# Kernel tuning notes

Hardware: AMD Instinct MI355X
Metric: run time of the kernel (lower is better)

The kernel has to match this reference:

```python
import jax, jax.numpy as jnp
import numpy as np

WIDTH_POW = 9
WIDTH = 2 ** WIDTH_POW          # 512
HALF = WIDTH // 2               # 256
DEPTH = 32
BATCH = 65536
EPS = 0.01


def setup_inputs() -> dict:
    key = jax.random.key(0)
    k1, k2, k3, k4, k5, k6 = jax.random.split(key, 6)
    X = jax.random.normal(k1, (BATCH, WIDTH), dtype=jnp.float32)
    # butterfly rotation angles, one stage of depth-1 butterfly per layer
    thetas = jax.random.uniform(k2, (DEPTH, HALF), dtype=jnp.float32) * (2.0 * np.pi)
    # SmoothBendActivation params, init uniform in [-eps, eps]
    def u(k):
        return jax.random.uniform(k, (DEPTH, WIDTH), dtype=jnp.float32) * (2 * EPS) - EPS
    biases = u(k3)
    slopes1 = u(k4)
    slopes2 = u(k5)
    curvatures = u(k6)
    return {"X": X, "thetas": thetas, "biases": biases,
            "slopes1": slopes1, "slopes2": slopes2, "curvatures": curvatures}


def reference(X, thetas, biases, slopes1, slopes2, curvatures):
    B = X.shape[0]

    def step(x, p):
        theta, bias, s1, s2, curv = p
        # --- orthogonal butterfly rotation (depth 1) ---
        c = jnp.cos(theta)  # [HALF]
        s = jnp.sin(theta)
        x0 = x[:, :HALF]
        x1 = x[:, HALF:]
        n0 = x0 * c + x1 * s
        n1 = -x0 * s + x1 * c
        # fixed permutation perm[2j] = j, perm[2j+1] = j + HALF: interleave n0, n1
        x = jnp.stack([n0, n1], axis=-1).reshape(B, WIDTH)
        # --- smooth bend activation ---
        m1 = jnp.exp(s1)
        m2 = jnp.exp(s2)
        a = (m1 + m2) * 0.5
        cc = (m2 - m1) / (2.0 * a)
        b = jnp.sinh(bias)
        k = jnp.exp(curv)
        u = x * a - b
        x = u + cc * jnp.sqrt(u * u + 1.0 / k)
        return x, None

    out, _ = jax.lax.scan(step, X, (thetas, biases, slopes1, slopes2, curvatures))
    return out  # num_outputs == WIDTH, so no final slice needed
```

## Files before the change

kernel.cpp:

```cpp
#include <hip/hip_runtime.h>
#include <math.h>

#define WIDTH 512
#define HALF  256
#define DEPTH 32
#define BATCH 65536
#define RPW   8

__device__ float4 g_T1[DEPTH * WIDTH];
__device__ float  g_T2[DEPTH * WIDTH];

__global__ __launch_bounds__(256) void precompute_kernel(
    const float* __restrict__ thetas, const float* __restrict__ biases,
    const float* __restrict__ slopes1, const float* __restrict__ slopes2,
    const float* __restrict__ curvatures) {
  int tid = blockIdx.x * 256 + threadIdx.x;
  if (tid >= DEPTH * WIDTH) return;
  int d = tid >> 9;
  int p = tid & 511;
  int rot = (d + 1) % 9;
  int j = ((p << rot) | (p >> (9 - rot))) & 511;
  int i = j >> 1;
  int role = j & 1;
  float th = thetas[d * HALF + i];
  float c = cosf(th), s = sinf(th);
  float m1 = expf(slopes1[d * WIDTH + j]);
  float m2 = expf(slopes2[d * WIDTH + j]);
  float a  = 0.5f * (m1 + m2);
  float cc = (m2 - m1) / (m1 + m2);
  float b  = sinhf(biases[d * WIDTH + j]);
  float invk = expf(-curvatures[d * WIDTH + j]);
  float A = a * c;
  float S = role ? (-a * s) : (a * s);
  int q = d * WIDTH + ((p & 7) * 64 + (p >> 3));
  g_T1[q] = make_float4(A, S, b, cc);
  g_T2[q] = invk;
}

#if __has_builtin(__builtin_amdgcn_sqrtf)
#define FAST_SQRT(x) __builtin_amdgcn_sqrtf(x)
#else
#define FAST_SQRT(x) sqrtf(x)
#endif

template <int M>
__device__ __forceinline__ float xshfl(float v) {
  if constexpr (M < 32) {
    constexpr int ctl = (M << 10) | 0x1F;
    return __int_as_float(__builtin_amdgcn_ds_swizzle(__float_as_int(v), ctl));
  } else {
    return __shfl_xor(v, 32, 64);
  }
}

__device__ __forceinline__ float stepf(float xs, float v, float4 P, float ik) {
  float u = fmaf(xs, P.x, fmaf(v, P.y, -P.z));
  float t = fmaf(u, u, ik);
  return fmaf(P.w, FAST_SQRT(t), u);
}

template <int K>
__device__ __forceinline__ void do_layer(const float4* __restrict__ t1,
                                         const float* __restrict__ t2,
                                         float (&x)[8][RPW]) {
  if constexpr (K >= 3) {
    constexpr int m = 1 << (K - 3);
#pragma unroll
    for (int s = 0; s < 8; ++s) {
      float4 P = t1[s * 64];
      float ik = t2[s * 64];
#pragma unroll
      for (int r = 0; r < RPW; ++r) {
        float xs = x[s][r];
        float v = xshfl<m>(xs);
        x[s][r] = stepf(xs, v, P, ik);
      }
    }
  } else {
    constexpr int SX = 1 << K;
#pragma unroll
    for (int s0 = 0; s0 < 8; ++s0) {
      if (s0 & SX) continue;
      const int s1 = s0 | SX;
      float4 P0 = t1[s0 * 64];
      float ik0 = t2[s0 * 64];
      float4 P1 = t1[s1 * 64];
      float ik1 = t2[s1 * 64];
#pragma unroll
      for (int r = 0; r < RPW; ++r) {
        float v0 = x[s0][r], v1 = x[s1][r];
        float n0 = stepf(v0, v1, P0, ik0);
        float n1 = stepf(v1, v0, P1, ik1);
        x[s0][r] = n0;
        x[s1][r] = n1;
      }
    }
  }
}

__global__ __launch_bounds__(256, 4) void net_kernel(const float* __restrict__ X,
                                                     float* __restrict__ out) {
  const int lane = threadIdx.x & 63;
  const int wv = blockIdx.x * 4 + (threadIdx.x >> 6);
  const size_t row0 = (size_t)wv * RPW;

  float x[8][RPW];
  const float4* __restrict__ Xv =
      reinterpret_cast<const float4*>(X + row0 * WIDTH);
#pragma unroll
  for (int r = 0; r < RPW; ++r) {
    float4 a = Xv[r * (WIDTH / 4) + lane * 2];
    float4 b = Xv[r * (WIDTH / 4) + lane * 2 + 1];
    x[0][r] = a.x; x[1][r] = a.y; x[2][r] = a.z; x[3][r] = a.w;
    x[4][r] = b.x; x[5][r] = b.y; x[6][r] = b.z; x[7][r] = b.w;
  }

#define RUN_LAYER(DD)                                                   \
  do {                                                                  \
    if (d0 + DD < DEPTH) {                                              \
      do_layer<8 - DD>(g_T1 + (d0 + DD) * WIDTH + lane,                 \
                       g_T2 + (d0 + DD) * WIDTH + lane, x);             \
    }                                                                   \
  } while (0)

  for (int d0 = 0; d0 < DEPTH; d0 += 9) {
    RUN_LAYER(0); RUN_LAYER(1); RUN_LAYER(2);
    RUN_LAYER(3); RUN_LAYER(4); RUN_LAYER(5);
    RUN_LAYER(6); RUN_LAYER(7); RUN_LAYER(8);
  }
#undef RUN_LAYER

  float* __restrict__ O = out + row0 * WIDTH;
#pragma unroll
  for (int s = 0; s < 8; ++s) {
    const int p = lane * 8 + s;
    const int cfin = ((p << 5) | (p >> 4)) & 511;
#pragma unroll
    for (int r = 0; r < RPW; ++r) O[r * WIDTH + cfin] = x[s][r];
  }
}

extern "C" void kernel_launch(void* const* d_in, const int* in_sizes, int n_in,
                              void* d_out, int out_size, void* d_ws, size_t ws_size,
                              hipStream_t stream) {
  const float* X          = (const float*)d_in[0];
  const float* thetas     = (const float*)d_in[1];
  const float* biases     = (const float*)d_in[2];
  const float* slopes1    = (const float*)d_in[3];
  const float* slopes2    = (const float*)d_in[4];
  const float* curvatures = (const float*)d_in[5];
  float* out = (float*)d_out;

  hipLaunchKernelGGL(precompute_kernel, dim3((DEPTH * WIDTH + 255) / 256),
                     dim3(256), 0, stream, thetas, biases, slopes1, slopes2,
                     curvatures);
  hipLaunchKernelGGL(net_kernel, dim3(BATCH / (RPW * 4)), dim3(256), 0, stream,
                     X, out);
}
```

Baseline: 202.5 us.

## Split each row across two wavefronts, exchanging via LDS for top bit

Each wavefront now holds 4 row elements per lane instead of 8. A 128-thread block covers one 8-row group, and the parameter table layout is remapped to match. The butterfly level that crosses wavefronts goes through shared memory with two __syncthreads per such layer. This halves register pressure per thread and doubles the wave count to improve occupancy and latency hiding, at the cost of LDS traffic and block barriers.

```diff
diff --git a/kernel.cpp b/kernel.cpp
--- a/kernel.cpp
+++ b/kernel.cpp
@@ -6,6 +6,7 @@
 #define DEPTH 32
 #define BATCH 65536
 #define RPW   8
+#define NS    4
 
 __device__ float4 g_T1[DEPTH * WIDTH];
 __device__ float  g_T2[DEPTH * WIDTH];
@@ -17,24 +18,25 @@
   int tid = blockIdx.x * 256 + threadIdx.x;
   if (tid >= DEPTH * WIDTH) return;
   int d = tid >> 9;
-  int p = tid & 511;
+  int idx = tid & 511;
+  int w = idx >> 8, s = (idx >> 6) & 3, l = idx & 63;
+  int p = w * 256 + l * 4 + s;
   int rot = (d + 1) % 9;
   int j = ((p << rot) | (p >> (9 - rot))) & 511;
   int i = j >> 1;
   int role = j & 1;
   float th = thetas[d * HALF + i];
-  float c = cosf(th), s = sinf(th);
+  float c = cosf(th), sn = sinf(th);
   float m1 = expf(slopes1[d * WIDTH + j]);
   float m2 = expf(slopes2[d * WIDTH + j]);
   float a  = 0.5f * (m1 + m2);
   float cc = (m2 - m1) / (m1 + m2);
   float b  = sinhf(biases[d * WIDTH + j]);
-  float invk = expf(-curvatures[d * WIDTH + j]);
+  float ik = expf(-curvatures[d * WIDTH + j]);
   float A = a * c;
-  float S = role ? (-a * s) : (a * s);
-  int q = d * WIDTH + ((p & 7) * 64 + (p >> 3));
-  g_T1[q] = make_float4(A, S, b, cc);
-  g_T2[q] = invk;
+  float S = role ? (-a * sn) : (a * sn);
+  g_T1[d * WIDTH + idx] = make_float4(A, S, b, cc);
+  g_T2[d * WIDTH + idx] = ik;
 }
 
 #if __has_builtin(__builtin_amdgcn_sqrtf)
@@ -60,13 +62,33 @@
 }
 
 template <int K>
-__device__ __forceinline__ void do_layer(const float4* __restrict__ t1,
-                                         const float* __restrict__ t2,
-                                         float (&x)[8][RPW]) {
-  if constexpr (K >= 3) {
-    constexpr int m = 1 << (K - 3);
+__device__ __forceinline__ void layer_step(const float4* __restrict__ t1,
+                                           const float* __restrict__ t2,
+                                           float (&x)[NS][RPW], float* xb,
+                                           int tid) {
+  if constexpr (K == 8) {
 #pragma unroll
-    for (int s = 0; s < 8; ++s) {
+    for (int s = 0; s < NS; ++s)
+#pragma unroll
+      for (int r = 0; r < RPW; ++r)
+        xb[(s * RPW + r) * 128 + tid] = x[s][r];
+    __syncthreads();
+    const int pt = tid ^ 64;
+#pragma unroll
+    for (int s = 0; s < NS; ++s) {
+      float4 P = t1[s * 64];
+      float ik = t2[s * 64];
+      float v[RPW];
+#pragma unroll
+      for (int r = 0; r < RPW; ++r) v[r] = xb[(s * RPW + r) * 128 + pt];
+#pragma unroll
+      for (int r = 0; r < RPW; ++r) x[s][r] = stepf(x[s][r], v[r], P, ik);
+    }
+    __syncthreads();
+  } else if constexpr (K >= 2) {
+    constexpr int m = 1 << (K - 2);
+#pragma unroll
+    for (int s = 0; s < NS; ++s) {
       float4 P = t1[s * 64];
       float ik = t2[s * 64];
 #pragma unroll
@@ -79,7 +101,7 @@
   } else {
     constexpr int SX = 1 << K;
 #pragma unroll
-    for (int s0 = 0; s0 < 8; ++s0) {
+    for (int s0 = 0; s0 < NS; ++s0) {
       if (s0 & SX) continue;
       const int s1 = s0 | SX;
       float4 P0 = t1[s0 * 64];
@@ -98,31 +120,32 @@
   }
 }
 
-__global__ __launch_bounds__(256, 4) void net_kernel(const float* __restrict__ X,
+__global__ __launch_bounds__(128, 4) void net_kernel(const float* __restrict__ X,
                                                      float* __restrict__ out) {
-  const int lane = threadIdx.x & 63;
-  const int wv = blockIdx.x * 4 + (threadIdx.x >> 6);
-  const size_t row0 = (size_t)wv * RPW;
+  __shared__ float xb[NS * RPW * 128];
+  const int tid = threadIdx.x;
+  const int lane = tid & 63;
+  const int w = tid >> 6;
+  const size_t row0 = (size_t)blockIdx.x * RPW;
 
-  float x[8][RPW];
-  const float4* __restrict__ Xv =
-      reinterpret_cast<const float4*>(X + row0 * WIDTH);
+  float x[NS][RPW];
+  const float* __restrict__ Xp = X + row0 * WIDTH + w * 256 + lane * 4;
 #pragma unroll
   for (int r = 0; r < RPW; ++r) {
-    float4 a = Xv[r * (WIDTH / 4) + lane * 2];
-    float4 b = Xv[r * (WIDTH / 4) + lane * 2 + 1];
+    float4 a = *reinterpret_cast<const float4*>(Xp + (size_t)r * WIDTH);
     x[0][r] = a.x; x[1][r] = a.y; x[2][r] = a.z; x[3][r] = a.w;
-    x[4][r] = b.x; x[5][r] = b.y; x[6][r] = b.z; x[7][r] = b.w;
   }
 
-#define RUN_LAYER(DD)                                                   \
-  do {                                                                  \
-    if (d0 + DD < DEPTH) {                                              \
-      do_layer<8 - DD>(g_T1 + (d0 + DD) * WIDTH + lane,                 \
-                       g_T2 + (d0 + DD) * WIDTH + lane, x);             \
-    }                                                                   \
+  const int poff = w * 256 + lane;
+#define RUN_LAYER(DD)                                                    \
+  do {                                                                   \
+    if (d0 + DD < DEPTH) {                                               \
+      layer_step<8 - DD>(g_T1 + (d0 + DD) * WIDTH + poff,                \
+                         g_T2 + (d0 + DD) * WIDTH + poff, x, xb, tid);   \
+    }                                                                    \
   } while (0)
 
+#pragma unroll 1
   for (int d0 = 0; d0 < DEPTH; d0 += 9) {
     RUN_LAYER(0); RUN_LAYER(1); RUN_LAYER(2);
     RUN_LAYER(3); RUN_LAYER(4); RUN_LAYER(5);
@@ -132,8 +155,8 @@
 
   float* __restrict__ O = out + row0 * WIDTH;
 #pragma unroll
-  for (int s = 0; s < 8; ++s) {
-    const int p = lane * 8 + s;
+  for (int s = 0; s < NS; ++s) {
+    const int p = w * 256 + lane * 4 + s;
     const int cfin = ((p << 5) | (p >> 4)) & 511;
 #pragma unroll
     for (int r = 0; r < RPW; ++r) O[r * WIDTH + cfin] = x[s][r];
@@ -154,6 +177,6 @@
   hipLaunchKernelGGL(precompute_kernel, dim3((DEPTH * WIDTH + 255) / 256),
                      dim3(256), 0, stream, thetas, biases, slopes1, slopes2,
                      curvatures);
-  hipLaunchKernelGGL(net_kernel, dim3(BATCH / (RPW * 4)), dim3(256), 0, stream,
+  hipLaunchKernelGGL(net_kernel, dim3(BATCH / RPW), dim3(128), 0, stream,
                      X, out);
 }
```

Result: no change. 201.6 us (-0.5%).
